# Optimization experiments

Measured on AMD Instinct MI355X. Metric: run time of the kernel, lower is better.

## Reference

```python
import jax, jax.numpy as jnp
import numpy as np

B, T, D, H, L, K = 64, 512, 256, 256, 2, 3


def setup_inputs() -> dict:
    key = jax.random.key(0)
    ks = jax.random.split(key, 12)
    s = 0.05
    f = jnp.float32
    return {
        "x": jax.random.normal(ks[0], (B, T, D), f),
        # GRUCell params per layer (torch gate order: r, z, n)
        "W_ih": jax.random.normal(ks[1], (L, 3 * H, H), f) * s,
        "b_ih": jax.random.normal(ks[2], (L, 3 * H), f) * s,
        "W_hh": jax.random.normal(ks[3], (L, 3 * H, H), f) * s,
        "b_hh": jax.random.normal(ks[4], (L, 3 * H), f) * s,
        # refinement cell params per layer
        "Wg": jax.random.normal(ks[5], (L, H, 2 * H), f) * s,
        "bg": jax.random.normal(ks[6], (L, H), f) * s,
        "Wt": jax.random.normal(ks[7], (L, H, 2 * H), f) * s,
        "bt": jax.random.normal(ks[8], (L, H), f) * s,
        "Wu": jax.random.normal(ks[9], (L, H, H), f) * s,
        "bu": jax.random.normal(ks[10], (L, H), f) * s,
    }


def reference(x, W_ih, b_ih, W_hh, b_hh, Wg, bg, Wt, bt, Wu, bu):
    def step(hidden, x_t):  # hidden: (L, B, H), x_t: (B, D)
        inp = x_t
        new_hiddens = []
        for l in range(L):
            h = hidden[l]
            # GRU cell (torch semantics)
            gi = inp @ W_ih[l].T + b_ih[l]
            gh = h @ W_hh[l].T + b_hh[l]
            i_r, i_z, i_n = jnp.split(gi, 3, axis=-1)
            h_r, h_z, h_n = jnp.split(gh, 3, axis=-1)
            r = jax.nn.sigmoid(i_r + h_r)
            z = jax.nn.sigmoid(i_z + h_z)
            n = jnp.tanh(i_n + r * h_n)
            h_new = (1.0 - z) * n + z * h
            # recursive refinement
            out = h_new
            rh = h_new
            for _ in range(K):
                comb = jnp.concatenate([out, rh], axis=-1)  # (B, 2H)
                g = jax.nn.sigmoid(comb @ Wg[l].T + bg[l])
                ref = jnp.tanh(comb @ Wt[l].T + bt[l])
                out = g * ref + (1.0 - g) * out
                rh = jnp.tanh(out @ Wu[l].T + bu[l])
            new_hiddens.append(h_new)
            inp = out
        return jnp.stack(new_hiddens, axis=0), inp

    hidden0 = jnp.zeros((L, B, H), x.dtype)
    final_hidden, outs = jax.lax.scan(step, hidden0, jnp.swapaxes(x, 0, 1))
    output = jnp.swapaxes(outs, 0, 1)  # (B, T, H)
    return output, final_hidden
```

## Files before the change

### kernel.cpp

```cpp
#include <hip/hip_runtime.h>

typedef float  f32x4  __attribute__((ext_vector_type(4)));
typedef __bf16 bf16x8 __attribute__((ext_vector_type(8)));

#define NB 64
#define NT 512
#define ND 256
#define NH 256
#define NROW (NB*NT)

#define OFF_WIH 0
#define OFF_WHH 393216
#define OFF_WGT 786432
#define OFF_WU  1310720
#define W_TOTAL 1441792
#define OFF_GI   (W_TOTAL)
#define OFF_OUT0 (OFF_GI + 512*64*768)
#define OFF_OUT1 (OFF_OUT0 + NROW*256)
#define OFF_FLAG (OFF_OUT1 + NROW*256)

#define NW 96

__device__ inline unsigned short f2bu(float f){
  unsigned int u = __builtin_bit_cast(unsigned int, f);
  unsigned int r = u + 0x7fffu + ((u >> 16) & 1u);
  return (unsigned short)(r >> 16);
}
__device__ inline float bf2f(unsigned short u){
  unsigned int v = ((unsigned int)u) << 16;
  return __builtin_bit_cast(float, v);
}
__device__ inline float sigm(float x){ return 1.0f / (1.0f + __expf(-x)); }
__device__ inline float tanhf_(float x){ return 1.0f - 2.0f / (__expf(2.0f * x) + 1.0f); }

#define MFMA(a,b,c) __builtin_amdgcn_mfma_f32_16x16x32_bf16((a),(b),(c),0,0,0)

__device__ inline void gload_lds16(const void* g, void* l){
  __builtin_amdgcn_global_load_lds(
    (const __attribute__((address_space(1))) unsigned int*)g,
    (__attribute__((address_space(3))) unsigned int*)l, 16, 0, 0);
}
__device__ inline bf16x8 ldG(const unsigned short* p){
  return *reinterpret_cast<const bf16x8*>(p);
}
template<int SLP>
__device__ inline void spin_ge(int* p, int tgt){
  while (__hip_atomic_load(p, __ATOMIC_RELAXED, __HIP_MEMORY_SCOPE_AGENT) < tgt)
    __builtin_amdgcn_s_sleep(SLP);
}

__global__ void cvt_weights(const float* __restrict__ Wih, const float* __restrict__ Whh,
                            const float* __restrict__ Wg,  const float* __restrict__ Wt,
                            const float* __restrict__ Wu,  unsigned short* __restrict__ ws){
  int i = blockIdx.x * blockDim.x + threadIdx.x;
  if (i < OFF_WHH) {
    ws[i] = f2bu(Wih[i]);
  } else if (i < OFF_WGT) {
    ws[i] = f2bu(Whh[i - OFF_WHH]);
  } else if (i < OFF_WU) {
    int j = i - OFF_WGT;
    int l = j >> 18; int r = (j >> 9) & 511; int k = j & 511;
    float v = (r < 256) ? Wg[(l * 256 + r) * 512 + k]
                        : Wt[(l * 256 + (r - 256)) * 512 + k];
    ws[i] = f2bu(v);
  } else if (i < W_TOTAL) {
    ws[i] = f2bu(Wu[i - OFF_WU]);
  }
}

__global__ void pack_x(const float* __restrict__ x, unsigned short* __restrict__ xin){
  size_t i = ((size_t)blockIdx.x * blockDim.x + threadIdx.x) * 4;
  float4 v = *reinterpret_cast<const float4*>(x + i);
  ushort4 u; u.x = f2bu(v.x); u.y = f2bu(v.y); u.z = f2bu(v.z); u.w = f2bu(v.w);
  *reinterpret_cast<ushort4*>(xin + i) = u;
}

__global__ __launch_bounds__(1024) void gi_gemm(
    const unsigned short* __restrict__ xin,
    const unsigned short* __restrict__ wih,
    const float* __restrict__ bih, const float* __restrict__ bhh,
    unsigned short* __restrict__ gi)
{
  __shared__ alignas(16) unsigned short sA[64 * 256];
  const int tid = threadIdx.x, blk = blockIdx.x;
  const int ln = tid & 63, wv = tid >> 6, m = ln & 15, lg = ln >> 4;
  {
    const char* src = (const char*)(xin + (size_t)blk * 64 * 256);
    #pragma unroll
    for (int i = 0; i < 2; ++i){
      int o = tid * 16 + i * 16384;
      int r = o >> 9, wb = o & 511;
      gload_lds16(src + (size_t)r * 512 + (wb ^ ((r & 7) << 4)), (char*)sA + o);
    }
  }
  __syncthreads();
  f32x4 acc[3][4] = {};
  #pragma unroll
  for (int kc = 0; kc < 8; ++kc){
    int kk = kc * 32 + lg * 8;
    bf16x8 a[4];
    #pragma unroll
    for (int mt = 0; mt < 4; ++mt){
      int row = mt * 16 + m;
      a[mt] = *(const bf16x8*)((const char*)sA + row * 512 + ((kk * 2) ^ ((row & 7) << 4)));
    }
    #pragma unroll
    for (int g = 0; g < 3; ++g){
      bf16x8 b = ldG(wih + (size_t)(g * 256 + wv * 16 + m) * 256 + kk);
      #pragma unroll
      for (int mt = 0; mt < 4; ++mt) acc[g][mt] = MFMA(a[mt], b, acc[g][mt]);
    }
  }
  const int c = wv * 16 + m;
  #pragma unroll
  for (int g = 0; g < 3; ++g){
    float bias = bih[g * 256 + c] + (g < 2 ? bhh[g * 256 + c] : 0.f);
    #pragma unroll
    for (int mt = 0; mt < 4; ++mt){
      #pragma unroll
      for (int j = 0; j < 4; ++j){
        int row = blk * 64 + mt * 16 + lg * 4 + j;
        int b = row >> 9, t = row & 511;
        gi[((size_t)t * 64 + b) * 768 + g * 256 + c] = f2bu(acc[g][mt][j] + bias);
      }
    }
  }
}

__device__ void chain_role(
    int grp, const unsigned short* __restrict__ gi, const unsigned short* __restrict__ whh,
    const float* __restrict__ bhh, unsigned short* __restrict__ outw,
    float* __restrict__ hfin, int* prog, int* bd, char* smem)
{
  __builtin_amdgcn_s_setprio(1);
  char* hAc = smem;
  const int tid = threadIdx.x;
  const int ln  = tid & 63, wv = tid >> 6;
  const int m   = ln & 15;
  const int lg  = ln >> 4;

  f32x4 wf[3][2][8];
  #pragma unroll
  for (int g = 0; g < 3; ++g)
    #pragma unroll
    for (int s = 0; s < 2; ++s){
      const unsigned short* p = whh + (size_t)(g * 256 + wv * 32 + s * 16 + m) * 256;
      #pragma unroll
      for (int kc = 0; kc < 8; ++kc){
        wf[g][s][kc] = *reinterpret_cast<const f32x4*>(p + kc * 32 + lg * 8);
        asm volatile("" : "+v"(wf[g][s][kc]));
      }
    }

  const int bb   = lg & 1;
  const int su   = lg >> 1;
  const int wcol = wv * 32 + su * 16 + m;
  const int brow = grp * 2 + bb;
  const float bNv = bhh[512 + wcol];

  const int arow  = m & 1;
  const int arows = arow << 4;
  const int rbase = arow * 512;
  const int wbyte = bb * 512 + ((wcol * 2) ^ (bb << 4));

  const unsigned short* gbase = gi + (size_t)brow * 768 + wcol;
  unsigned short* op = outw + (size_t)brow * NT * 256 + wcol;

  if (tid < 256){
    ((unsigned int*)hAc)[tid] = 0;
    ((unsigned int*)(hAc + 1024))[tid] = 0;
  }
  if (bd){
    if (tid == 0){ spin_ge<8>(&bd[0], 16); spin_ge<8>(&bd[1], 16); __threadfence(); }
    __syncthreads();
    (void)__hip_atomic_load(&bd[0], __ATOMIC_ACQUIRE, __HIP_MEMORY_SCOPE_AGENT);
  }
  unsigned int gAr = gbase[0], gAz = gbase[256], gAn = gbase[512];
  unsigned int gBr = gbase[49152], gBz = gbase[49152 + 256], gBn = gbase[49152 + 512];
  float h = 0.f;
  __syncthreads();

  auto body = [&](int t, int curo, unsigned int& GR, unsigned int& GZ, unsigned int& GN){
    float xr = bf2f((unsigned short)GR);
    float xz = bf2f((unsigned short)GZ);
    float xn = bf2f((unsigned short)GN);
    if (t + 2 < NT){
      const unsigned short* gp = gbase + (size_t)(t + 2) * 49152;
      GR = gp[0]; GZ = gp[256]; GN = gp[512];
    }
    f32x4 a00{}, a01{}, a10{}, a11{}, a20{}, a21{};
    #pragma unroll
    for (int kc = 0; kc < 8; ++kc){
      int kb = kc * 64 + lg * 16;
      bf16x8 hv = *(const bf16x8*)(hAc + curo + rbase + (kb ^ arows));
      a00 = MFMA(hv, __builtin_bit_cast(bf16x8, wf[0][0][kc]), a00);
      a01 = MFMA(hv, __builtin_bit_cast(bf16x8, wf[0][1][kc]), a01);
      a10 = MFMA(hv, __builtin_bit_cast(bf16x8, wf[1][0][kc]), a10);
      a11 = MFMA(hv, __builtin_bit_cast(bf16x8, wf[1][1][kc]), a11);
      a20 = MFMA(hv, __builtin_bit_cast(bf16x8, wf[2][0][kc]), a20);
      a21 = MFMA(hv, __builtin_bit_cast(bf16x8, wf[2][1][kc]), a21);
    }
    float aR = su ? (bb ? a01[1] : a01[0]) : (bb ? a00[1] : a00[0]);
    float aZ = su ? (bb ? a11[1] : a11[0]) : (bb ? a10[1] : a10[0]);
    float aN = su ? (bb ? a21[1] : a21[0]) : (bb ? a20[1] : a20[0]);
    float R = sigm(aR + xr);
    float Z = sigm(aZ + xz);
    float N = tanhf_(xn + R * (aN + bNv));
    h = N + Z * (h - N);
    unsigned short hb = f2bu(h);
    *(unsigned short*)(hAc + (curo ^ 1024) + wbyte) = hb;
    op[t * 256] = hb;
    asm volatile("s_waitcnt lgkmcnt(0)" ::: "memory");
    __builtin_amdgcn_sched_barrier(0);
    __builtin_amdgcn_s_barrier();
    __builtin_amdgcn_sched_barrier(0);
  };

  for (int tp = 0; tp < NT; tp += 2){
    if ((tp & 15) == 0){
      if (tp > 0){
        __syncthreads();
        if (tid == 0){
          __threadfence();
          __hip_atomic_store(prog, tp, __ATOMIC_RELEASE, __HIP_MEMORY_SCOPE_AGENT);
        }
      }
      if (bd){
        int B1 = (tp >> 4) + 1;
        if (B1 < 32){
          if (tid == 0){ spin_ge<8>(&bd[B1], 16); __threadfence(); }
          __syncthreads();
          (void)__hip_atomic_load(&bd[B1], __ATOMIC_ACQUIRE, __HIP_MEMORY_SCOPE_AGENT);
        }
      }
    }
    body(tp,     0,    gAr, gAz, gAn);
    body(tp + 1, 1024, gBr, gBz, gBn);
  }
  __syncthreads();
  if (tid == 0){
    __threadfence();
    __hip_atomic_store(prog, NT, __ATOMIC_RELEASE, __HIP_MEMORY_SCOPE_AGENT);
  }
  hfin[(size_t)brow * 256 + wcol] = h;
}

__device__ void worker_role(
    int w, unsigned short* __restrict__ gi,
    const unsigned short* __restrict__ outw0, const unsigned short* __restrict__ outw1,
    const unsigned short* __restrict__ wsb,
    const float* __restrict__ bih, const float* __restrict__ bhh,
    const float* __restrict__ bg, const float* __restrict__ bt, const float* __restrict__ bu,
    float* __restrict__ o, int* flags, char* smem)
{
  const int tid = threadIdx.x;
  const int ln = tid & 63, wv = tid >> 6, m = ln & 15, lg = ln >> 4;

  auto ldA = [&](int row, int kbyte) -> bf16x8 {
    return *(const bf16x8*)(smem + row * 1024 + (kbyte ^ ((row & 7) << 4)));
  };

  for (int i = w; i < 1024; i += NW){
    const int lay = i >> 9, t = i & 511;
    int* prog = &flags[lay * 32];
    if (tid == 0){
      for (int q = 0; q < 32; ++q) spin_ge<32>(&prog[q], t + 1);
      __threadfence();
    }
    __syncthreads();
    (void)__hip_atomic_load(&prog[0], __ATOMIC_ACQUIRE, __HIP_MEMORY_SCOPE_AGENT);

    const unsigned short* src0 = lay ? outw1 : outw0;
    #pragma unroll
    for (int q = 0; q < 8; ++q){
      int ofs = tid * 16 + q * 8192;
      int r = ofs >> 10, wb = ofs & 1023;
      int wb2 = (wb ^ ((r & 7) << 4)) & 511;
      gload_lds16((const char*)(src0 + ((size_t)r * NT + t) * 256) + wb2, smem + ofs);
    }
    __syncthreads();

    const unsigned short* wgt = wsb + OFF_WGT + (size_t)lay * 512 * 512;
    const unsigned short* wu  = wsb + OFF_WU  + (size_t)lay * 256 * 256;
    const float* bgp = bg + lay * 256;
    const float* btp = bt + lay * 256;
    const float* bup = bu + lay * 256;

    for (int iter = 0; iter < 3; ++iter){
      float oo0[4][4], oo1[4][4];
      {
        f32x4 ag[4] = {}, at4[4] = {};
        #pragma unroll 2
        for (int kc = 0; kc < 16; ++kc){
          int kk = kc * 32 + lg * 8;
          bf16x8 Bg = ldG(wgt + (size_t)(      wv * 32 + m) * 512 + kk);
          bf16x8 Bt = ldG(wgt + (size_t)(256 + wv * 32 + m) * 512 + kk);
          #pragma unroll
          for (int mt = 0; mt < 4; ++mt){
            bf16x8 A = ldA(mt * 16 + m, kk * 2);
            ag[mt]  = MFMA(A, Bg, ag[mt]);
            at4[mt] = MFMA(A, Bt, at4[mt]);
          }
        }
        int col = wv * 32 + m;
        float bgv = bgp[col], btv = btp[col];
        #pragma unroll
        for (int mt = 0; mt < 4; ++mt)
          #pragma unroll
          for (int j = 0; j < 4; ++j){
            int row = mt * 16 + lg * 4 + j;
            float old = bf2f(*(unsigned short*)(smem + row * 1024 + ((col * 2) ^ ((row & 7) << 4))));
            float g  = sigm(ag[mt][j] + bgv);
            float rf = tanhf_(at4[mt][j] + btv);
            oo0[mt][j] = g * rf + (1.f - g) * old;
          }
      }
      {
        f32x4 ag[4] = {}, at4[4] = {};
        #pragma unroll 2
        for (int kc = 0; kc < 16; ++kc){
          int kk = kc * 32 + lg * 8;
          bf16x8 Bg = ldG(wgt + (size_t)(      wv * 32 + 16 + m) * 512 + kk);
          bf16x8 Bt = ldG(wgt + (size_t)(256 + wv * 32 + 16 + m) * 512 + kk);
          #pragma unroll
          for (int mt = 0; mt < 4; ++mt){
            bf16x8 A = ldA(mt * 16 + m, kk * 2);
            ag[mt]  = MFMA(A, Bg, ag[mt]);
            at4[mt] = MFMA(A, Bt, at4[mt]);
          }
        }
        int col = wv * 32 + 16 + m;
        float bgv = bgp[col], btv = btp[col];
        #pragma unroll
        for (int mt = 0; mt < 4; ++mt)
          #pragma unroll
          for (int j = 0; j < 4; ++j){
            int row = mt * 16 + lg * 4 + j;
            float old = bf2f(*(unsigned short*)(smem + row * 1024 + ((col * 2) ^ ((row & 7) << 4))));
            float g  = sigm(ag[mt][j] + bgv);
            float rf = tanhf_(at4[mt][j] + btv);
            oo1[mt][j] = g * rf + (1.f - g) * old;
          }
      }
      __syncthreads();
      if (iter == 2 && lay == 1){
        #pragma unroll
        for (int mt = 0; mt < 4; ++mt)
          #pragma unroll
          for (int j = 0; j < 4; ++j){
            int b = mt * 16 + lg * 4 + j;
            o[((size_t)b * NT + t) * 256 + wv * 32 + m]      = oo0[mt][j];
            o[((size_t)b * NT + t) * 256 + wv * 32 + 16 + m] = oo1[mt][j];
          }
      } else {
        #pragma unroll
        for (int mt = 0; mt < 4; ++mt)
          #pragma unroll
          for (int j = 0; j < 4; ++j){
            int row = mt * 16 + lg * 4 + j;
            int c0 = wv * 32 + m, c1 = wv * 32 + 16 + m;
            *(unsigned short*)(smem + row * 1024 + ((c0 * 2) ^ ((row & 7) << 4))) = f2bu(oo0[mt][j]);
            *(unsigned short*)(smem + row * 1024 + ((c1 * 2) ^ ((row & 7) << 4))) = f2bu(oo1[mt][j]);
          }
        __syncthreads();
        if (iter < 2){
          #pragma unroll
          for (int s = 0; s < 2; ++s){
            f32x4 au[4] = {};
            #pragma unroll
            for (int kc = 0; kc < 8; ++kc){
              int kk = kc * 32 + lg * 8;
              bf16x8 Bu = ldG(wu + (size_t)(wv * 32 + s * 16 + m) * 256 + kk);
              #pragma unroll
              for (int mt = 0; mt < 4; ++mt)
                au[mt] = MFMA(ldA(mt * 16 + m, kk * 2), Bu, au[mt]);
            }
            int col = wv * 32 + s * 16 + m;
            float buv = bup[col];
            #pragma unroll
            for (int mt = 0; mt < 4; ++mt)
              #pragma unroll
              for (int j = 0; j < 4; ++j){
                int row = mt * 16 + lg * 4 + j;
                *(unsigned short*)(smem + row * 1024 + (((512 + col * 2)) ^ ((row & 7) << 4)))
                    = f2bu(tanhf_(au[mt][j] + buv));
              }
          }
          __syncthreads();
        }
      }
    }
    if (lay == 0){
      const unsigned short* wih1 = wsb + OFF_WIH + (size_t)768 * 256;
      #pragma unroll
      for (int q = 0; q < 6; ++q){
        int tile = wv + 8 * q;
        int cg = tile * 16 + m;
        f32x4 acc[4] = {};
        #pragma unroll
        for (int kc = 0; kc < 8; ++kc){
          int kk = kc * 32 + lg * 8;
          bf16x8 B = ldG(wih1 + (size_t)cg * 256 + kk);
          #pragma unroll
          for (int mt = 0; mt < 4; ++mt)
            acc[mt] = MFMA(ldA(mt * 16 + m, kk * 2), B, acc[mt]);
        }
        float bias = bih[768 + cg] + (cg < 512 ? bhh[768 + cg] : 0.f);
        #pragma unroll
        for (int mt = 0; mt < 4; ++mt)
          #pragma unroll
          for (int j = 0; j < 4; ++j){
            int b = mt * 16 + lg * 4 + j;
            gi[((size_t)t * 64 + b) * 768 + cg] = f2bu(acc[mt][j] + bias);
          }
      }
      __syncthreads();
      if (tid == 0){
        __threadfence();
        __hip_atomic_fetch_add(&flags[64 + (t >> 4)], 1, __ATOMIC_RELEASE, __HIP_MEMORY_SCOPE_AGENT);
      }
    } else {
      __syncthreads();
    }
  }
}

__global__ __launch_bounds__(512, 2) void mega(
    unsigned short* __restrict__ gi, const unsigned short* __restrict__ wsb,
    const float* __restrict__ bih, const float* __restrict__ bhh,
    const float* __restrict__ bg, const float* __restrict__ bt, const float* __restrict__ bu,
    unsigned short* __restrict__ outw0, unsigned short* __restrict__ outw1,
    float* __restrict__ o, float* __restrict__ hf, int* flags)
{
  __shared__ char smem[65536];
  const int role = blockIdx.x;
  if (role < NW){
    worker_role(role, gi, outw0, outw1, wsb, bih, bhh, bg, bt, bu, o, flags, smem);
  } else if (role < NW + 32){
    chain_role(role - NW, gi, wsb + OFF_WHH, bhh, outw0, hf,
               &flags[role - NW], nullptr, smem);
  } else {
    chain_role(role - NW - 32, gi, wsb + OFF_WHH + 768 * 256, bhh + 768, outw1,
               hf + 64 * 256, &flags[32 + (role - NW - 32)], &flags[64], smem);
  }
}

extern "C" void kernel_launch(void* const* d_in, const int* in_sizes, int n_in,
                              void* d_out, int out_size, void* d_ws, size_t ws_size,
                              hipStream_t stream) {
  const float* x   = (const float*)d_in[0];
  const float* Wih = (const float*)d_in[1];
  const float* bih = (const float*)d_in[2];
  const float* Whh = (const float*)d_in[3];
  const float* bhh = (const float*)d_in[4];
  const float* Wg  = (const float*)d_in[5];
  const float* bg  = (const float*)d_in[6];
  const float* Wt  = (const float*)d_in[7];
  const float* bt  = (const float*)d_in[8];
  const float* Wu  = (const float*)d_in[9];
  const float* bu  = (const float*)d_in[10];
  unsigned short* ws = (unsigned short*)d_ws;
  float* o  = (float*)d_out;
  float* hf = o + (size_t)NB * NT * NH;

  unsigned short* gi    = ws + OFF_GI;
  unsigned short* outw0 = ws + OFF_OUT0;
  unsigned short* outw1 = ws + OFF_OUT1;
  unsigned short* xin   = ws + OFF_OUT1;
  int* flags = (int*)(ws + OFF_FLAG);

  cvt_weights<<<W_TOTAL / 256, 256, 0, stream>>>(Wih, Whh, Wg, Wt, Wu, ws);
  pack_x<<<(NROW * 256 / 4) / 256, 256, 0, stream>>>(x, xin);
  gi_gemm<<<512, 1024, 0, stream>>>(xin, ws + OFF_WIH, bih, bhh, gi);
  (void)hipMemsetAsync(flags, 0, 96 * sizeof(int), stream);
  mega<<<NW + 64, 512, 0, stream>>>(gi, ws, bih, bhh, bg, bt, bu, outw0, outw1, o, hf, flags);
}
```

Before: 1.221 ms.

## Fuse column halves in refinement GEMMs to reuse A fragments and double worker blocks

Merges the two sequential 16-column passes of the gate/transform, update and layer-1 input-projection GEMMs into single loops. Each A fragment is loaded from LDS once and feeds twice as many MFMAs, and the loads are hoisted ahead of the MFMA chain. The worker count NW is also raised from 96 to 192, changing how the refinement work is spread across blocks. In exchange, more accumulators are live per thread, which raises register pressure under launch_bounds(512,2), and the extra blocks may contend for CU resources.

After: 979.3 us, median of 2. 19.8% less time.

```diff
diff --git a/kernel.cpp b/kernel.cpp
--- a/kernel.cpp
+++ b/kernel.cpp
@@ -19,7 +19,7 @@
 #define OFF_OUT1 (OFF_OUT0 + NROW*256)
 #define OFF_FLAG (OFF_OUT1 + NROW*256)
 
-#define NW 96
+#define NW 192
 
 __device__ inline unsigned short f2bu(float f){
   unsigned int u = __builtin_bit_cast(unsigned int, f);
@@ -289,57 +289,40 @@
     for (int iter = 0; iter < 3; ++iter){
       float oo0[4][4], oo1[4][4];
       {
-        f32x4 ag[4] = {}, at4[4] = {};
+        f32x4 ag0[4] = {}, at0[4] = {}, ag1[4] = {}, at1[4] = {};
         #pragma unroll 2
         for (int kc = 0; kc < 16; ++kc){
           int kk = kc * 32 + lg * 8;
-          bf16x8 Bg = ldG(wgt + (size_t)(      wv * 32 + m) * 512 + kk);
-          bf16x8 Bt = ldG(wgt + (size_t)(256 + wv * 32 + m) * 512 + kk);
+          bf16x8 A[4];
+          #pragma unroll
+          for (int mt = 0; mt < 4; ++mt) A[mt] = ldA(mt * 16 + m, kk * 2);
+          bf16x8 Bg0 = ldG(wgt + (size_t)(      wv * 32 + m) * 512 + kk);
+          bf16x8 Bt0 = ldG(wgt + (size_t)(256 + wv * 32 + m) * 512 + kk);
+          bf16x8 Bg1 = ldG(wgt + (size_t)(      wv * 32 + 16 + m) * 512 + kk);
+          bf16x8 Bt1 = ldG(wgt + (size_t)(256 + wv * 32 + 16 + m) * 512 + kk);
           #pragma unroll
           for (int mt = 0; mt < 4; ++mt){
-            bf16x8 A = ldA(mt * 16 + m, kk * 2);
-            ag[mt]  = MFMA(A, Bg, ag[mt]);
-            at4[mt] = MFMA(A, Bt, at4[mt]);
+            ag0[mt] = MFMA(A[mt], Bg0, ag0[mt]);
+            at0[mt] = MFMA(A[mt], Bt0, at0[mt]);
+            ag1[mt] = MFMA(A[mt], Bg1, ag1[mt]);
+            at1[mt] = MFMA(A[mt], Bt1, at1[mt]);
           }
         }
-        int col = wv * 32 + m;
-        float bgv = bgp[col], btv = btp[col];
+        int c0 = wv * 32 + m, c1 = wv * 32 + 16 + m;
+        float bg0 = bgp[c0], bt0 = btp[c0], bg1 = bgp[c1], bt1 = btp[c1];
         #pragma unroll
         for (int mt = 0; mt < 4; ++mt)
           #pragma unroll
           for (int j = 0; j < 4; ++j){
             int row = mt * 16 + lg * 4 + j;
-            float old = bf2f(*(unsigned short*)(smem + row * 1024 + ((col * 2) ^ ((row & 7) << 4))));
-            float g  = sigm(ag[mt][j] + bgv);
-            float rf = tanhf_(at4[mt][j] + btv);
-            oo0[mt][j] = g * rf + (1.f - g) * old;
-          }
-      }
-      {
-        f32x4 ag[4] = {}, at4[4] = {};
-        #pragma unroll 2
-        for (int kc = 0; kc < 16; ++kc){
-          int kk = kc * 32 + lg * 8;
-          bf16x8 Bg = ldG(wgt + (size_t)(      wv * 32 + 16 + m) * 512 + kk);
-          bf16x8 Bt = ldG(wgt + (size_t)(256 + wv * 32 + 16 + m) * 512 + kk);
-          #pragma unroll
-          for (int mt = 0; mt < 4; ++mt){
-            bf16x8 A = ldA(mt * 16 + m, kk * 2);
-            ag[mt]  = MFMA(A, Bg, ag[mt]);
-            at4[mt] = MFMA(A, Bt, at4[mt]);
-          }
-        }
-        int col = wv * 32 + 16 + m;
-        float bgv = bgp[col], btv = btp[col];
-        #pragma unroll
-        for (int mt = 0; mt < 4; ++mt)
-          #pragma unroll
-          for (int j = 0; j < 4; ++j){
-            int row = mt * 16 + lg * 4 + j;
-            float old = bf2f(*(unsigned short*)(smem + row * 1024 + ((col * 2) ^ ((row & 7) << 4))));
-            float g  = sigm(ag[mt][j] + bgv);
-            float rf = tanhf_(at4[mt][j] + btv);
-            oo1[mt][j] = g * rf + (1.f - g) * old;
+            float old0 = bf2f(*(unsigned short*)(smem + row * 1024 + ((c0 * 2) ^ ((row & 7) << 4))));
+            float old1 = bf2f(*(unsigned short*)(smem + row * 1024 + ((c1 * 2) ^ ((row & 7) << 4))));
+            float g0 = sigm(ag0[mt][j] + bg0);
+            float r0 = tanhf_(at0[mt][j] + bt0);
+            float g1 = sigm(ag1[mt][j] + bg1);
+            float r1 = tanhf_(at1[mt][j] + bt1);
+            oo0[mt][j] = g0 * r0 + (1.f - g0) * old0;
+            oo1[mt][j] = g1 * r1 + (1.f - g1) * old1;
           }
       }
       __syncthreads();
@@ -364,28 +347,33 @@
           }
         __syncthreads();
         if (iter < 2){
-          #pragma unroll
-          for (int s = 0; s < 2; ++s){
-            f32x4 au[4] = {};
+          f32x4 au0[4] = {}, au1[4] = {};
+          #pragma unroll 2
+          for (int kc = 0; kc < 8; ++kc){
+            int kk = kc * 32 + lg * 8;
+            bf16x8 A[4];
             #pragma unroll
-            for (int kc = 0; kc < 8; ++kc){
-              int kk = kc * 32 + lg * 8;
-              bf16x8 Bu = ldG(wu + (size_t)(wv * 32 + s * 16 + m) * 256 + kk);
-              #pragma unroll
-              for (int mt = 0; mt < 4; ++mt)
-                au[mt] = MFMA(ldA(mt * 16 + m, kk * 2), Bu, au[mt]);
+            for (int mt = 0; mt < 4; ++mt) A[mt] = ldA(mt * 16 + m, kk * 2);
+            bf16x8 Bu0 = ldG(wu + (size_t)(wv * 32 + m) * 256 + kk);
+            bf16x8 Bu1 = ldG(wu + (size_t)(wv * 32 + 16 + m) * 256 + kk);
+            #pragma unroll
+            for (int mt = 0; mt < 4; ++mt){
+              au0[mt] = MFMA(A[mt], Bu0, au0[mt]);
+              au1[mt] = MFMA(A[mt], Bu1, au1[mt]);
             }
-            int col = wv * 32 + s * 16 + m;
-            float buv = bup[col];
+          }
+          int c0 = wv * 32 + m, c1 = wv * 32 + 16 + m;
+          float bu0 = bup[c0], bu1 = bup[c1];
+          #pragma unroll
+          for (int mt = 0; mt < 4; ++mt)
             #pragma unroll
-            for (int mt = 0; mt < 4; ++mt)
-              #pragma unroll
-              for (int j = 0; j < 4; ++j){
-                int row = mt * 16 + lg * 4 + j;
-                *(unsigned short*)(smem + row * 1024 + (((512 + col * 2)) ^ ((row & 7) << 4)))
-                    = f2bu(tanhf_(au[mt][j] + buv));
-              }
-          }
+            for (int j = 0; j < 4; ++j){
+              int row = mt * 16 + lg * 4 + j;
+              *(unsigned short*)(smem + row * 1024 + (((512 + c0 * 2)) ^ ((row & 7) << 4)))
+                  = f2bu(tanhf_(au0[mt][j] + bu0));
+              *(unsigned short*)(smem + row * 1024 + (((512 + c1 * 2)) ^ ((row & 7) << 4)))
+                  = f2bu(tanhf_(au1[mt][j] + bu1));
+            }
           __syncthreads();
         }
       }
@@ -393,25 +381,33 @@
     if (lay == 0){
       const unsigned short* wih1 = wsb + OFF_WIH + (size_t)768 * 256;
       #pragma unroll
-      for (int q = 0; q < 6; ++q){
-        int tile = wv + 8 * q;
-        int cg = tile * 16 + m;
-        f32x4 acc[4] = {};
+      for (int qp = 0; qp < 3; ++qp){
+        int cg0 = (wv + 8 * (2 * qp)) * 16 + m;
+        int cg1 = (wv + 8 * (2 * qp + 1)) * 16 + m;
+        f32x4 acc0[4] = {}, acc1[4] = {};
         #pragma unroll
         for (int kc = 0; kc < 8; ++kc){
           int kk = kc * 32 + lg * 8;
-          bf16x8 B = ldG(wih1 + (size_t)cg * 256 + kk);
-          #pragma unroll
-          for (int mt = 0; mt < 4; ++mt)
-            acc[mt] = MFMA(ldA(mt * 16 + m, kk * 2), B, acc[mt]);
+          bf16x8 A[4];
+          #pragma unroll
+          for (int mt = 0; mt < 4; ++mt) A[mt] = ldA(mt * 16 + m, kk * 2);
+          bf16x8 B0 = ldG(wih1 + (size_t)cg0 * 256 + kk);
+          bf16x8 B1 = ldG(wih1 + (size_t)cg1 * 256 + kk);
+          #pragma unroll
+          for (int mt = 0; mt < 4; ++mt){
+            acc0[mt] = MFMA(A[mt], B0, acc0[mt]);
+            acc1[mt] = MFMA(A[mt], B1, acc1[mt]);
+          }
         }
-        float bias = bih[768 + cg] + (cg < 512 ? bhh[768 + cg] : 0.f);
+        float b0 = bih[768 + cg0] + (cg0 < 512 ? bhh[768 + cg0] : 0.f);
+        float b1 = bih[768 + cg1] + (cg1 < 512 ? bhh[768 + cg1] : 0.f);
         #pragma unroll
         for (int mt = 0; mt < 4; ++mt)
           #pragma unroll
           for (int j = 0; j < 4; ++j){
             int b = mt * 16 + lg * 4 + j;
-            gi[((size_t)t * 64 + b) * 768 + cg] = f2bu(acc[mt][j] + bias);
+            gi[((size_t)t * 64 + b) * 768 + cg0] = f2bu(acc0[mt][j] + b0);
+            gi[((size_t)t * 64 + b) * 768 + cg1] = f2bu(acc1[mt][j] + b1);
           }
       }
       __syncthreads();
```
